# Kernel tuning notes

Hardware: AMD Instinct MI355X
Metric: run time of the kernel (lower is better)

The kernel has to match this reference:

```python
import jax, jax.numpy as jnp
import numpy as np

N = 50000   # nodes
E = 800000  # edges (avg degree 16)
D = 128     # input feature dim
H = 128     # hidden dim
C = 10      # num classes
G = 16      # graphs in batch


def setup_inputs() -> dict:
    key = jax.random.key(0)
    ks = jax.random.split(key, 12)
    def w(k, shape):
        return jax.random.normal(k, shape, jnp.float32) / np.sqrt(shape[0]).astype(np.float32)
    return {
        "h": jax.random.normal(ks[0], (N, D), jnp.float32),
        "src": jax.random.randint(ks[1], (E,), 0, N, jnp.int32),
        "dst": jax.random.randint(ks[2], (E,), 0, N, jnp.int32),
        "graph_ids": jnp.sort(jax.random.randint(ks[3], (N,), 0, G, jnp.int32)),
        "W1a": w(ks[4], (D, H)), "b1a": jnp.zeros((H,), jnp.float32),
        "W2a": w(ks[5], (H, H)), "b2a": jnp.zeros((H,), jnp.float32),
        "W1b": w(ks[6], (H, H)), "b1b": jnp.zeros((H,), jnp.float32),
        "W2b": w(ks[7], (H, H)), "b2b": jnp.zeros((H,), jnp.float32),
        "Wc1": w(ks[8], (H, H)), "bc1": jnp.zeros((H,), jnp.float32),
        "Wc2": w(ks[9], (H, C)), "bc2": jnp.zeros((C,), jnp.float32),
    }


def _gin_layer(h, src, dst, W1, b1, W2, b2):
    # GIN aggregation, eps=0: z_i = h_i + sum_{j in N(i)} h_j
    agg = jax.ops.segment_sum(h[src], dst, num_segments=N)
    z = h + agg
    # 2-layer MLP apply function with relu activation ('relu' arg of GINLayer)
    z = jax.nn.relu(z @ W1 + b1)
    return jax.nn.relu(z @ W2 + b2)


def reference(h, src, dst, graph_ids, W1a, b1a, W2a, b2a,
              W1b, b1b, W2b, b2b, Wc1, bc1, Wc2, bc2):
    h = _gin_layer(h, src, dst, W1a, b1a, W2a, b2a)   # [N, H]
    h = _gin_layer(h, src, dst, W1b, b1b, W2b, b2b)   # [N, H]
    # dgl.mean_nodes over the batched graph
    sums = jax.ops.segment_sum(h, graph_ids, num_segments=G)                # [G, H]
    cnts = jax.ops.segment_sum(jnp.ones((N, 1), h.dtype), graph_ids, num_segments=G)
    h_g = sums / jnp.maximum(cnts, 1.0)
    # cls MLP: linear -> relu -> linear (logits)
    out = jax.nn.relu(h_g @ Wc1 + bc1) @ Wc2 + bc2    # [G, C]
    return out
```

## Files before the change

### kernel.cpp

```cpp
#include <hip/hip_runtime.h>
#include <stdint.h>

#define NN 50000
#define EE 800000
#define DD 128
#define GG 16
#define CC 10
#define NBK 196
#define BCH 4096
#define SMAX 5120
#define FT (NBK * NBK)
#define NSCN ((FT + 255) / 256)

typedef unsigned short u16;
typedef __bf16 bf16x8 __attribute__((ext_vector_type(8)));
typedef float f32x4 __attribute__((ext_vector_type(4)));
typedef unsigned int u32x4 __attribute__((ext_vector_type(4)));
typedef float fl4 __attribute__((ext_vector_type(4)));

__device__ inline u16 f2bf(float f) {
    unsigned u = __float_as_uint(f);
    u = u + 0x7fffu + ((u >> 16) & 1u);
    return (u16)(u >> 16);
}
__device__ inline unsigned pack2(float a, float b) {
    return (unsigned)f2bf(a) | ((unsigned)f2bf(b) << 16);
}
__device__ inline float bf2f(unsigned bits16) { return __uint_as_float(bits16 << 16); }
__device__ inline void acc8(float* a, uint4 v) {
    a[0] += __uint_as_float(v.x << 16); a[1] += __uint_as_float(v.x & 0xffff0000u);
    a[2] += __uint_as_float(v.y << 16); a[3] += __uint_as_float(v.y & 0xffff0000u);
    a[4] += __uint_as_float(v.z << 16); a[5] += __uint_as_float(v.z & 0xffff0000u);
    a[6] += __uint_as_float(v.w << 16); a[7] += __uint_as_float(v.w & 0xffff0000u);
}
__device__ inline void mand(uint4& v, int p) {
    unsigned m = p ? 0xffffffffu : 0u;
    v.x &= m; v.y &= m; v.z &= m; v.w &= m;
}
__device__ inline void nt_store16(void* p, uint4 v) {
    u32x4 x; x.x = v.x; x.y = v.y; x.z = v.z; x.w = v.w;
    __builtin_nontemporal_store(x, (u32x4*)p);
}
__device__ inline uint4 nt_load16(const void* p) {
    u32x4 x = __builtin_nontemporal_load((const u32x4*)p);
    uint4 r; r.x = x.x; r.y = x.y; r.z = x.z; r.w = x.w;
    return r;
}
__device__ inline float4 nt_loadf4(const float* p) {
    fl4 x = __builtin_nontemporal_load((const fl4*)p);
    float4 r; r.x = x.x; r.y = x.y; r.z = x.z; r.w = x.w;
    return r;
}

#define PZ (GG * DD)
#define PC (NN * DD / 4)
#define PW (4 * DD * DD)
#define PTOT (PZ + PC + PW)
#define PBLK ((PTOT + 255) / 256)

__global__ __launch_bounds__(256) void prepsort_kernel(
    const float* __restrict__ h,
    const float* __restrict__ a, const float* __restrict__ b,
    const float* __restrict__ c, const float* __restrict__ d,
    int* __restrict__ zbase, u16* __restrict__ H0, u16* __restrict__ wt,
    const int* __restrict__ dst, int* __restrict__ counts) {
    __shared__ int hist[NBK];
    int blk = blockIdx.x, t = threadIdx.x;
    if (blk < NBK) {
        for (int i = t; i < NBK; i += 256) hist[i] = 0;
        __syncthreads();
        int e0 = blk * BCH, e1 = min(e0 + BCH, EE);
        for (int e = e0 + t; e < e1; e += 256) atomicAdd(&hist[dst[e] >> 8], 1);
        __syncthreads();
        for (int i = t; i < NBK; i += 256) counts[i * NBK + blk] = hist[i];
        return;
    }
    int i = (blk - NBK) * 256 + t;
    if (i < PZ) { zbase[i] = 0; return; }
    i -= PZ;
    if (i < PC) {
        int j = i * 4;
        float4 v = nt_loadf4(h + j);
        ushort4 o;
        o.x = f2bf(v.x); o.y = f2bf(v.y); o.z = f2bf(v.z); o.w = f2bf(v.w);
        *(ushort4*)(H0 + j) = o;
        return;
    }
    i -= PC;
    if (i < PW) {
        int m = i >> 14, r = i & 16383, k = r >> 7, j = r & 127;
        const float* W = (m == 0) ? a : (m == 1) ? b : (m == 2) ? c : d;
        wt[(m << 14) + (j << 7) + k] = f2bf(W[(k << 7) + j]);
    }
}

__global__ __launch_bounds__(256) void scanA_kernel(int* __restrict__ counts,
                                                    int* __restrict__ bsum) {
    __shared__ int tmp[256];
    int t = threadIdx.x, idx = blockIdx.x * 256 + t;
    int v = (idx < FT) ? counts[idx] : 0;
    tmp[t] = v; __syncthreads();
    for (int off = 1; off < 256; off <<= 1) {
        int x = (t >= off) ? tmp[t - off] : 0;
        __syncthreads();
        tmp[t] += x;
        __syncthreads();
    }
    if (idx < FT) counts[idx] = tmp[t] - v;
    if (t == 255) bsum[blockIdx.x] = tmp[255];
}

__global__ __launch_bounds__(256) void scanB_kernel(int* __restrict__ bsum,
                                                    const int* __restrict__ gids,
                                                    int* __restrict__ gstart) {
    __shared__ int tmp[256];
    int t = threadIdx.x;
    if (t <= GG) {
        int lo = 0, hi = NN;
        while (lo < hi) { int mid = (lo + hi) >> 1; if (gids[mid] < t) lo = mid + 1; else hi = mid; }
        gstart[t] = lo;
    }
    int v = (t < NSCN) ? bsum[t] : 0;
    tmp[t] = v; __syncthreads();
    for (int off = 1; off < 256; off <<= 1) {
        int x = (t >= off) ? tmp[t - off] : 0;
        __syncthreads();
        tmp[t] += x;
        __syncthreads();
    }
    if (t < NSCN) bsum[t] = tmp[t] - v;
}

__global__ __launch_bounds__(256) void scanC_kernel(int* __restrict__ counts,
                                                    const int* __restrict__ bsum) {
    int idx = blockIdx.x * 256 + threadIdx.x;
    if (idx < FT) counts[idx] += bsum[blockIdx.x];
}

__global__ __launch_bounds__(256) void sortP3_kernel(const int* __restrict__ src,
                                                     const int* __restrict__ dst,
                                                     const int* __restrict__ counts,
                                                     int* __restrict__ epack) {
    __shared__ int curs[NBK];
    int b = blockIdx.x, t = threadIdx.x;
    for (int i = t; i < NBK; i += 256) curs[i] = counts[i * NBK + b];
    __syncthreads();
    int e0 = b * BCH, e1 = min(e0 + BCH, EE);
    for (int e = e0 + t; e < e1; e += 256) {
        int dd = dst[e], s = src[e];
        int p = atomicAdd(&curs[dd >> 8], 1);
        epack[p] = (s << 8) | (dd & 255);
    }
}

__global__ __launch_bounds__(256) void sortP4_kernel(const int* __restrict__ epack,
                                                     const int* __restrict__ counts,
                                                     int* __restrict__ offs,
                                                     int* __restrict__ ssrc) {
    __shared__ int hist[256];
    __shared__ int curs[256];
    __shared__ int stage[SMAX];
    int j = blockIdx.x, t = threadIdx.x;
    int n0 = j << 8;
    int b0 = counts[j * NBK];
    int b1 = (j < NBK - 1) ? counts[(j + 1) * NBK] : EE;
    hist[t] = 0;
    __syncthreads();
    for (int e = b0 + t; e < b1; e += 256) atomicAdd(&hist[epack[e] & 255], 1);
    __syncthreads();
    int deg = hist[t];
    for (int off = 1; off < 256; off <<= 1) {
        int x = (t >= off) ? hist[t - off] : 0;
        __syncthreads();
        hist[t] += x;
        __syncthreads();
    }
    int loff = hist[t] - deg;
    curs[t] = loff;
    if (n0 + t <= NN) offs[n0 + t] = b0 + loff;
    __syncthreads();
    for (int e = b0 + t; e < b1; e += 256) {
        int pk = epack[e];
        int p = atomicAdd(&curs[pk & 255], 1);
        stage[p] = pk >> 8;
    }
    __syncthreads();
    int n = b1 - b0;
    for (int i = t; i < n; i += 256) ssrc[b0 + i] = stage[i];
}

__global__ __launch_bounds__(256) void agg_kernel(
    const u16* __restrict__ Hin, const int* __restrict__ offs,
    const int* __restrict__ ssrc, u16* __restrict__ Z) {
    int gid = blockIdx.x * 32 + (threadIdx.x >> 3);
    int lid = threadIdx.x & 7;
    if (gid >= 2 * NN) return;
    int node = gid >> 1;
    int foff = (gid & 1) * 64 + lid * 8;
    const u16* base = Hin + foff;

    float acc[8] = {0.f, 0.f, 0.f, 0.f, 0.f, 0.f, 0.f, 0.f};
    uint4 vs = *(const uint4*)(base + (size_t)node * DD);
    int e0 = offs[node], e1 = offs[node + 1];
    acc8(acc, vs);

    int nch = (e1 - e0 + 7) >> 3;
    if (nch > 0) {
        int elast = e1 - 1;
        int i0 = ssrc[e0];
        int i1 = ssrc[min(e0 + 1, elast)];
        int i2 = ssrc[min(e0 + 2, elast)];
        int i3 = ssrc[min(e0 + 3, elast)];
        int i4 = ssrc[min(e0 + 4, elast)];
        int i5 = ssrc[min(e0 + 5, elast)];
        int i6 = ssrc[min(e0 + 6, elast)];
        int i7 = ssrc[min(e0 + 7, elast)];
        int eb = e0;
        for (int c = 0; c < nch; c++) {
            int ebn = eb + 8;
            int n0 = i0, n1 = i1, n2 = i2, n3 = i3, n4 = i4, n5 = i5, n6 = i6, n7 = i7;
            if (c + 1 < nch) {
                n0 = ssrc[ebn];
                n1 = ssrc[min(ebn + 1, elast)];
                n2 = ssrc[min(ebn + 2, elast)];
                n3 = ssrc[min(ebn + 3, elast)];
                n4 = ssrc[min(ebn + 4, elast)];
                n5 = ssrc[min(ebn + 5, elast)];
                n6 = ssrc[min(ebn + 6, elast)];
                n7 = ssrc[min(ebn + 7, elast)];
            }
            uint4 v0 = *(const uint4*)(base + (size_t)i0 * DD);
            uint4 v1 = *(const uint4*)(base + (size_t)i1 * DD);
            uint4 v2 = *(const uint4*)(base + (size_t)i2 * DD);
            uint4 v3 = *(const uint4*)(base + (size_t)i3 * DD);
            uint4 v4 = *(const uint4*)(base + (size_t)i4 * DD);
            uint4 v5 = *(const uint4*)(base + (size_t)i5 * DD);
            uint4 v6 = *(const uint4*)(base + (size_t)i6 * DD);
            uint4 v7 = *(const uint4*)(base + (size_t)i7 * DD);
            mand(v1, eb + 1 < e1); mand(v2, eb + 2 < e1); mand(v3, eb + 3 < e1);
            mand(v4, eb + 4 < e1); mand(v5, eb + 5 < e1); mand(v6, eb + 6 < e1);
            mand(v7, eb + 7 < e1);
            acc8(acc, v0); acc8(acc, v1); acc8(acc, v2); acc8(acc, v3);
            acc8(acc, v4); acc8(acc, v5); acc8(acc, v6); acc8(acc, v7);
            i0 = n0; i1 = n1; i2 = n2; i3 = n3; i4 = n4; i5 = n5; i6 = n6; i7 = n7;
            eb = ebn;
        }
    }
    uint4 o;
    o.x = pack2(acc[0], acc[1]); o.y = pack2(acc[2], acc[3]);
    o.z = pack2(acc[4], acc[5]); o.w = pack2(acc[6], acc[7]);
    nt_store16(Z + (size_t)node * DD + foff, o);
}

__global__ __launch_bounds__(256) void mlp_kernel(
    const u16* __restrict__ Zin, const u16* __restrict__ Wt1, const float* __restrict__ b1,
    const u16* __restrict__ Wt2, const float* __restrict__ b2,
    u16* __restrict__ Hout) {
    __shared__ u16 zb[64][136];
    const int wave = threadIdx.x >> 6;
    const int lane = threadIdx.x & 63;
    const int m16 = lane & 15;
    const int quad = lane >> 4;
    const int row0 = blockIdx.x * 64 + wave * 16;

#pragma unroll
    for (int p = 0; p < 4; p++) {
        int idx = p * 64 + lane;
        int r = idx >> 4, ch = idx & 15;
        if (row0 + r < NN) {
            uint4 v = nt_load16(Zin + (size_t)(row0 + r) * DD + ch * 8);
            *(uint4*)&zb[wave * 16 + r][ch * 8] = v;
        }
    }

    bf16x8 afr[4];
#pragma unroll
    for (int kk = 0; kk < 4; kk++)
        afr[kk] = *(const bf16x8*)&zb[wave * 16 + m16][kk * 32 + quad * 8];
    f32x4 acc[8];
#pragma unroll
    for (int nt = 0; nt < 8; nt++) acc[nt] = (f32x4){0.f, 0.f, 0.f, 0.f};
#pragma unroll
    for (int kk = 0; kk < 4; kk++) {
#pragma unroll
        for (int nt = 0; nt < 8; nt++) {
            bf16x8 bfr = *(const bf16x8*)(Wt1 + ((nt * 16 + m16) << 7) + kk * 32 + quad * 8);
            acc[nt] = __builtin_amdgcn_mfma_f32_16x16x32_bf16(afr[kk], bfr, acc[nt], 0, 0, 0);
        }
    }
#pragma unroll
    for (int nt = 0; nt < 8; nt++) {
        int col = nt * 16 + m16;
        float bias = b1[col];
#pragma unroll
        for (int r = 0; r < 4; r++) {
            float yv = acc[nt][r] + bias;
            yv = yv > 0.f ? yv : 0.f;
            zb[wave * 16 + quad * 4 + r][col] = f2bf(yv);
        }
    }

#pragma unroll
    for (int kk = 0; kk < 4; kk++)
        afr[kk] = *(const bf16x8*)&zb[wave * 16 + m16][kk * 32 + quad * 8];
#pragma unroll
    for (int nt = 0; nt < 8; nt++) acc[nt] = (f32x4){0.f, 0.f, 0.f, 0.f};
#pragma unroll
    for (int kk = 0; kk < 4; kk++) {
#pragma unroll
        for (int nt = 0; nt < 8; nt++) {
            bf16x8 bfr = *(const bf16x8*)(Wt2 + ((nt * 16 + m16) << 7) + kk * 32 + quad * 8);
            acc[nt] = __builtin_amdgcn_mfma_f32_16x16x32_bf16(afr[kk], bfr, acc[nt], 0, 0, 0);
        }
    }
#pragma unroll
    for (int nt = 0; nt < 8; nt++) {
        int col = nt * 16 + m16;
        float bias = b2[col];
#pragma unroll
        for (int r = 0; r < 4; r++) {
            float ov = acc[nt][r] + bias;
            ov = ov > 0.f ? ov : 0.f;
            zb[wave * 16 + quad * 4 + r][col] = f2bf(ov);
        }
    }
#pragma unroll
    for (int p = 0; p < 4; p++) {
        int idx = p * 64 + lane;
        int r = idx >> 4, ch = idx & 15;
        if (row0 + r < NN)
            nt_store16(Hout + (size_t)(row0 + r) * DD + ch * 8, *(const uint4*)&zb[wave * 16 + r][ch * 8]);
    }
}

__global__ void pool_kernel(const u16* __restrict__ H2, const int* __restrict__ gstart,
                            float* __restrict__ pool) {
    int g = blockIdx.x >> 5, q = blockIdx.x & 31;
    int f = threadIdx.x;
    int s = gstart[g], e = gstart[g + 1];
    float sum = 0.f;
    for (int n = s + q; n < e; n += 32) sum += bf2f(H2[(size_t)n * DD + f]);
    atomicAdd(&pool[g * DD + f], sum);
}

__global__ void cls_kernel(const float* __restrict__ pool, const int* __restrict__ gstart,
                           const float* __restrict__ Wc1, const float* __restrict__ bc1,
                           const float* __restrict__ Wc2, const float* __restrict__ bc2,
                           float* __restrict__ out) {
    __shared__ float hg[128];
    __shared__ float y1[128];
    int g = blockIdx.x;
    int t = threadIdx.x;
    int cnt = gstart[g + 1] - gstart[g];
    float inv = 1.f / (float)(cnt > 1 ? cnt : 1);
    hg[t] = pool[g * DD + t] * inv;
    __syncthreads();
    float a = bc1[t];
    for (int k = 0; k < DD; k++) a += hg[k] * Wc1[k * DD + t];
    y1[t] = a > 0.f ? a : 0.f;
    __syncthreads();
    if (t < CC) {
        float o = bc2[t];
        for (int k = 0; k < DD; k++) o += y1[k] * Wc2[k * CC + t];
        out[g * CC + t] = o;
    }
}

extern "C" void kernel_launch(void* const* d_in, const int* in_sizes, int n_in,
                              void* d_out, int out_size, void* d_ws, size_t ws_size,
                              hipStream_t stream) {
    const float* h    = (const float*)d_in[0];
    const int*   src  = (const int*)d_in[1];
    const int*   dst  = (const int*)d_in[2];
    const int*   gids = (const int*)d_in[3];
    const float* W1a  = (const float*)d_in[4];
    const float* b1a  = (const float*)d_in[5];
    const float* W2a  = (const float*)d_in[6];
    const float* b2a  = (const float*)d_in[7];
    const float* W1b  = (const float*)d_in[8];
    const float* b1b  = (const float*)d_in[9];
    const float* W2b  = (const float*)d_in[10];
    const float* b2b  = (const float*)d_in[11];
    const float* Wc1  = (const float*)d_in[12];
    const float* bc1  = (const float*)d_in[13];
    const float* Wc2  = (const float*)d_in[14];
    const float* bc2  = (const float*)d_in[15];
    float* out = (float*)d_out;

    char* ws = (char*)d_ws;
    u16*   H0     = (u16*)(ws);
    u16*   H1     = (u16*)(ws + 12800000);
    u16*   H2     = (u16*)(ws + 25600000);
    u16*   Wt     = (u16*)(ws + 38400000);
    float* pool   = (float*)(ws + 38531072);
    int*   offs   = (int*)(ws + 38539264);
    int*   ssrc   = (int*)(ws + 38739268);
    int*   gstart = (int*)(ws + 41939268);
    int*   counts = (int*)(ws + 41939336);
    int*   bsum   = (int*)(ws + 42093000);
    int*   epack  = (int*)(ws + 42093792);
    u16*   Z1     = H2;
    u16*   Z2     = H0;

    prepsort_kernel<<<dim3(NBK + PBLK), dim3(256), 0, stream>>>(
        h, W1a, W2a, W1b, W2b, (int*)pool, H0, Wt, dst, counts);
    scanA_kernel<<<dim3(NSCN), dim3(256), 0, stream>>>(counts, bsum);
    scanB_kernel<<<dim3(1), dim3(256), 0, stream>>>(bsum, gids, gstart);
    scanC_kernel<<<dim3(NSCN), dim3(256), 0, stream>>>(counts, bsum);
    sortP3_kernel<<<dim3(NBK), dim3(256), 0, stream>>>(src, dst, counts, epack);
    sortP4_kernel<<<dim3(NBK), dim3(256), 0, stream>>>(epack, counts, offs, ssrc);
    agg_kernel<<<dim3((2 * NN + 31) / 32), dim3(256), 0, stream>>>(H0, offs, ssrc, Z1);
    mlp_kernel<<<dim3((NN + 63) / 64), dim3(256), 0, stream>>>(Z1, Wt, b1a, Wt + 16384, b2a, H1);
    agg_kernel<<<dim3((2 * NN + 31) / 32), dim3(256), 0, stream>>>(H1, offs, ssrc, Z2);
    mlp_kernel<<<dim3((NN + 63) / 64), dim3(256), 0, stream>>>(Z2, Wt + 32768, b1b, Wt + 49152, b2b, H2);
    pool_kernel<<<dim3(GG * 32), dim3(128), 0, stream>>>(H2, gstart, pool);
    cls_kernel<<<dim3(GG), dim3(128), 0, stream>>>(pool, gstart, Wc1, bc1, Wc2, bc2, out);
}
```

Measured before the change: 302.9 us.

## Stage bucket scatter through LDS and fuse mean-pool into second MLP

The bucket scatter pass now builds a per-block local histogram and prefix scan, scatters packed edges into a shared-memory buffer, then writes them to global memory contiguously per bucket instead of scattering directly. Separately, the graph mean-pool reduction is folded into the epilogue of the second MLP kernel, which sums its tile's rows per graph id and atomically adds into the pool buffer, removing the separate pool kernel and its re-read of H2. The scatter gains extra LDS work, a binary search per element and 16KB of shared memory that may lower occupancy. The fused pool adds a sync and serial per-column loops to every MLP block.

```diff
diff --git a/kernel.cpp b/kernel.cpp
--- a/kernel.cpp
+++ b/kernel.cpp
@@ -141,15 +141,45 @@
                                                      const int* __restrict__ dst,
                                                      const int* __restrict__ counts,
                                                      int* __restrict__ epack) {
-    __shared__ int curs[NBK];
+    __shared__ int lhist[NBK + 1];
+    __shared__ int lcur[NBK];
+    __shared__ int goff[NBK];
+    __shared__ int tmp[256];
+    __shared__ int sbuf[BCH];
     int b = blockIdx.x, t = threadIdx.x;
-    for (int i = t; i < NBK; i += 256) curs[i] = counts[i * NBK + b];
-    __syncthreads();
-    int e0 = b * BCH, e1 = min(e0 + BCH, EE);
+    int e0 = b * BCH, e1 = min(e0 + BCH, EE), n = e1 - e0;
+
+    for (int i = t; i < NBK; i += 256) lhist[i] = 0;
+    __syncthreads();
+    for (int e = e0 + t; e < e1; e += 256) atomicAdd(&lhist[dst[e] >> 8], 1);
+    __syncthreads();
+    int v = (t < NBK) ? lhist[t] : 0;
+    tmp[t] = v; __syncthreads();
+    for (int off = 1; off < 256; off <<= 1) {
+        int x = (t >= off) ? tmp[t - off] : 0;
+        __syncthreads();
+        tmp[t] += x;
+        __syncthreads();
+    }
+    if (t < NBK) {
+        int excl = tmp[t] - v;
+        lcur[t] = excl;
+        lhist[t] = excl;
+        goff[t] = counts[t * NBK + b] - excl;
+    }
+    if (t == 0) lhist[NBK] = n;
+    __syncthreads();
     for (int e = e0 + t; e < e1; e += 256) {
         int dd = dst[e], s = src[e];
-        int p = atomicAdd(&curs[dd >> 8], 1);
-        epack[p] = (s << 8) | (dd & 255);
+        int p = atomicAdd(&lcur[dd >> 8], 1);
+        sbuf[p] = (s << 8) | (dd & 255);
+    }
+    __syncthreads();
+    for (int i = t; i < n; i += 256) {
+        int pk = sbuf[i];
+        int lo = 0, hi = NBK - 1;
+        while (lo < hi) { int mid = (lo + hi + 1) >> 1; if (lhist[mid] <= i) lo = mid; else hi = mid - 1; }
+        epack[goff[lo] + i] = pk;
     }
 }
 
@@ -255,13 +285,18 @@
 __global__ __launch_bounds__(256) void mlp_kernel(
     const u16* __restrict__ Zin, const u16* __restrict__ Wt1, const float* __restrict__ b1,
     const u16* __restrict__ Wt2, const float* __restrict__ b2,
-    u16* __restrict__ Hout) {
+    u16* __restrict__ Hout, const int* __restrict__ gids, float* __restrict__ pool) {
     __shared__ u16 zb[64][136];
-    const int wave = threadIdx.x >> 6;
-    const int lane = threadIdx.x & 63;
+    __shared__ int garr[64];
+    const int tid = threadIdx.x;
+    const int wave = tid >> 6;
+    const int lane = tid & 63;
     const int m16 = lane & 15;
     const int quad = lane >> 4;
     const int row0 = blockIdx.x * 64 + wave * 16;
+    const int brow0 = blockIdx.x * 64;
+
+    if (pool && tid < 64) garr[tid] = (brow0 + tid < NN) ? gids[brow0 + tid] : 0;
 
 #pragma unroll
     for (int p = 0; p < 4; p++) {
@@ -331,16 +366,21 @@
         if (row0 + r < NN)
             nt_store16(Hout + (size_t)(row0 + r) * DD + ch * 8, *(const uint4*)&zb[wave * 16 + r][ch * 8]);
     }
-}
-
-__global__ void pool_kernel(const u16* __restrict__ H2, const int* __restrict__ gstart,
-                            float* __restrict__ pool) {
-    int g = blockIdx.x >> 5, q = blockIdx.x & 31;
-    int f = threadIdx.x;
-    int s = gstart[g], e = gstart[g + 1];
-    float sum = 0.f;
-    for (int n = s + q; n < e; n += 32) sum += bf2f(H2[(size_t)n * DD + f]);
-    atomicAdd(&pool[g * DD + f], sum);
+
+    if (pool) {
+        __syncthreads();
+        if (tid < DD) {
+            int cur = garr[0];
+            float s = 0.f;
+            for (int r = 0; r < 64; r++) {
+                if (brow0 + r >= NN) break;
+                int g = garr[r];
+                if (g != cur) { atomicAdd(&pool[cur * DD + tid], s); s = 0.f; cur = g; }
+                s += bf2f((unsigned)zb[r][tid]);
+            }
+            atomicAdd(&pool[cur * DD + tid], s);
+        }
+    }
 }
 
 __global__ void cls_kernel(const float* __restrict__ pool, const int* __restrict__ gstart,
@@ -410,9 +450,8 @@
     sortP3_kernel<<<dim3(NBK), dim3(256), 0, stream>>>(src, dst, counts, epack);
     sortP4_kernel<<<dim3(NBK), dim3(256), 0, stream>>>(epack, counts, offs, ssrc);
     agg_kernel<<<dim3((2 * NN + 31) / 32), dim3(256), 0, stream>>>(H0, offs, ssrc, Z1);
-    mlp_kernel<<<dim3((NN + 63) / 64), dim3(256), 0, stream>>>(Z1, Wt, b1a, Wt + 16384, b2a, H1);
+    mlp_kernel<<<dim3((NN + 63) / 64), dim3(256), 0, stream>>>(Z1, Wt, b1a, Wt + 16384, b2a, H1, gids, nullptr);
     agg_kernel<<<dim3((2 * NN + 31) / 32), dim3(256), 0, stream>>>(H1, offs, ssrc, Z2);
-    mlp_kernel<<<dim3((NN + 63) / 64), dim3(256), 0, stream>>>(Z2, Wt + 32768, b1b, Wt + 49152, b2b, H2);
-    pool_kernel<<<dim3(GG * 32), dim3(128), 0, stream>>>(H2, gstart, pool);
+    mlp_kernel<<<dim3((NN + 63) / 64), dim3(256), 0, stream>>>(Z2, Wt + 32768, b1b, Wt + 49152, b2b, H2, gids, pool);
     cls_kernel<<<dim3(GG), dim3(128), 0, stream>>>(pool, gstart, Wc1, bc1, Wc2, bc2, out);
 }
```

Result: faster. 280.2 us (-7.5%).
